# Optimization experiments

Measured on AMD Instinct MI355X. Metric: run time of the kernel, lower is better.

Reference implementation:

```python
import jax, jax.numpy as jnp
from jax import lax
import numpy as np

B, S, MEL = 64, 1024, 60
H, L = 180, 4
FS = 3          # mel_smooth_filter_size (num shifted conv branches)
BLOCKS = 3      # mel_smooth_layers
G = MEL // FS   # 20 output units per grouped conv
POST, OUT = 8192, 300


def setup_inputs() -> dict:
    key = jax.random.key(0)
    ks = jax.random.split(key, 13)
    rn = lambda k, shape, s: jax.random.normal(k, shape, jnp.float32) * s
    x = jax.random.normal(ks[0], (B, S, MEL), jnp.float32)
    lens = jax.random.randint(ks[1], (B,), 1, S + 1)
    conv_w = rn(ks[2], (BLOCKS, FS, G, FS, 5), 0.2)   # per block, per shift: (O=20, I/g=3, k=5)
    conv_b = rn(ks[3], (BLOCKS, FS, G), 0.1)
    lstm_wih0 = rn(ks[4], (4 * H, MEL), 0.08)
    lstm_wih_rest = rn(ks[5], (L - 1, 4 * H, H), 0.08)
    lstm_whh = rn(ks[6], (L, 4 * H, H), 0.08)
    lstm_bih = rn(ks[7], (L, 4 * H), 0.05)
    lstm_bhh = rn(ks[8], (L, 4 * H), 0.05)
    post_w = rn(ks[9], (POST, H), 0.05)
    post_b = rn(ks[10], (POST,), 0.05)
    up_w = rn(ks[11], (OUT, POST), 0.02)
    up_b = rn(ks[12], (OUT,), 0.02)
    return dict(x=x, lens=lens, conv_w=conv_w, conv_b=conv_b,
                lstm_wih0=lstm_wih0, lstm_wih_rest=lstm_wih_rest, lstm_whh=lstm_whh,
                lstm_bih=lstm_bih, lstm_bhh=lstm_bhh,
                post_w=post_w, post_b=post_b, up_w=up_w, up_b=up_b)


def _mel_block(xc, w, b):
    # xc: (B, MEL, S); w: (FS, G, FS, 5); b: (FS, G)
    zrow = jnp.zeros_like(xc[:, :1])
    xs = []
    for i in range(FS - 2):  # shift channels down by i+1
        n = i + 1
        xs.append(jnp.concatenate([jnp.zeros_like(xc[:, :n]), xc[:, :-n]], axis=1))
    xs.append(xc)
    xs.append(jnp.concatenate([xc[:, 1:], zrow], axis=1))  # shift channels up by 1
    outs = []
    for j in range(FS):
        o = lax.conv_general_dilated(xs[j], w[j], (1,), [(2, 2)],
                                     dimension_numbers=('NCH', 'OIH', 'NCH'),
                                     feature_group_count=G)
        outs.append(o + b[j][None, :, None])  # (B, G, S)
    # interleave: out channel FS*i + j = outs[j][:, i]
    return jnp.stack(outs, axis=2).reshape(xc.shape[0], MEL, xc.shape[2])


def _lstm_layer(h_in, wih, whh, bih, bhh):
    # h_in: (B, T, I). Torch gate order: i, f, g, o.
    pre = jnp.einsum('bti,gi->btg', h_in, wih) + (bih + bhh)  # (B, T, 4H)
    pre = pre.transpose(1, 0, 2)  # (T, B, 4H)
    h0 = jnp.zeros((h_in.shape[0], H), h_in.dtype)

    def step(carry, p):
        hh, cc = carry
        gates = p + hh @ whh.T
        i, f, g, o = jnp.split(gates, 4, axis=-1)
        cc = jax.nn.sigmoid(f) * cc + jax.nn.sigmoid(i) * jnp.tanh(g)
        hh = jax.nn.sigmoid(o) * jnp.tanh(cc)
        return (hh, cc), hh

    _, outs = lax.scan(step, (h0, h0), pre)
    return outs.transpose(1, 0, 2)  # (B, T, H)


def reference(x, lens, conv_w, conv_b, lstm_wih0, lstm_wih_rest, lstm_whh,
              lstm_bih, lstm_bhh, post_w, post_b, up_w, up_b):
    xc = x.transpose(0, 2, 1)  # (B, MEL, S)
    for blk in range(BLOCKS):
        shortcut = xc
        xc = _mel_block(xc, conv_w[blk], conv_b[blk]) + shortcut  # resid activation = Identity
    h = xc.transpose(0, 2, 1)  # (B, S, MEL)
    for l in range(L):
        wih = lstm_wih0 if l == 0 else lstm_wih_rest[l - 1]
        h = _lstm_layer(h, wih, lstm_whh[l], lstm_bih[l], lstm_bhh[l])
    idx = jnp.clip(lens - 1, 0, S - 1)
    last = h[jnp.arange(h.shape[0]), idx]  # (B, H)
    post = jax.nn.leaky_relu(last @ post_w.T + post_b, 0.01)  # LeakyReLU default slope
    return post @ up_w.T + up_b  # (B, OUT)
```

## Files before the change

### kernel.cpp

```cpp
#include <hip/hip_runtime.h>
#include <hip/hip_fp16.h>

#define BB 64
#define SS 1024
#define MEL 60
#define HH 180
#define G4 720
#define G4P 768
#define NCG 48
#define NKS 6
#define KP 192
#define NL 4
#define NPOST 8192
#define NOUT 300
#define NOUTP 320
#define KSPL 16
#define TT 128
#define CH 64
#define NCH (SS / CH)
#define KPAIR 96

typedef _Float16 f16x8 __attribute__((ext_vector_type(8)));
typedef float f32x4 __attribute__((ext_vector_type(4)));

#if defined(__has_builtin)
#if __has_builtin(__builtin_amdgcn_fdot2)
#define HAVE_FDOT2 1
#endif
#endif
#ifndef HAVE_FDOT2
#define HAVE_FDOT2 0
#endif

__device__ __forceinline__ float fdot2u(unsigned int w, unsigned int h, float acc) {
#if HAVE_FDOT2
    typedef _Float16 h2_t __attribute__((ext_vector_type(2)));
    union U { unsigned int u; h2_t v; };
    U a, b;
    a.u = w; b.u = h;
    return __builtin_amdgcn_fdot2(a.v, b.v, acc, false);
#else
    __half2 aw = *reinterpret_cast<const __half2*>(&w);
    __half2 ah = *reinterpret_cast<const __half2*>(&h);
    acc += __half2float(__low2half(aw)) * __half2float(__low2half(ah));
    acc += __half2float(__high2half(aw)) * __half2float(__high2half(ah));
    return acc;
#endif
}

union WU { uint4 u; f16x8 f; };

__global__ void prep_wmf(const float* __restrict__ whh, uint4* __restrict__ wmf) {
    int idx = blockIdx.x * blockDim.x + threadIdx.x;
    int total = NL * NCG * NKS * 64;
    if (idx >= total) return;
    int l = idx / (NCG * NKS * 64);
    int r = idx % (NCG * NKS * 64);
    int cg = r / (NKS * 64);
    int r2 = r % (NKS * 64);
    int ks = r2 / 64, lane = r2 % 64;
    int col = cg * 16 + (lane & 15);
    unsigned short v[8];
    #pragma unroll
    for (int j = 0; j < 8; ++j) {
        int k = ks * 32 + ((lane >> 4) << 3) + j;
        float f = (k < HH && col < G4) ? whh[((size_t)l * G4 + col) * HH + k] : 0.f;
        v[j] = __half_as_ushort(__float2half(f));
    }
    uint4 u;
    u.x = (unsigned)v[0] | ((unsigned)v[1] << 16);
    u.y = (unsigned)v[2] | ((unsigned)v[3] << 16);
    u.z = (unsigned)v[4] | ((unsigned)v[5] << 16);
    u.w = (unsigned)v[6] | ((unsigned)v[7] << 16);
    wmf[idx] = u;
}

__global__ void prep_wih16(const float* __restrict__ wih0, const float* __restrict__ wih_rest,
                           unsigned int* __restrict__ w) {
    int idx = blockIdx.x * blockDim.x + threadIdx.x;
    int total = NL * G4 * KPAIR;
    if (idx >= total) return;
    int l = idx / (G4 * KPAIR);
    int r = idx % (G4 * KPAIR);
    int g = r / KPAIR, kp = r % KPAIR;
    int K = (l == 0) ? MEL : HH;
    const float* src = (l == 0) ? (wih0 + (size_t)g * MEL)
                                : (wih_rest + ((size_t)(l - 1) * G4 + g) * HH);
    float a = 0.f, b = 0.f;
    if (2 * kp < K) { a = src[2 * kp]; b = src[2 * kp + 1]; }
    __half2 h2 = __floats2half2_rn(a, b);
    w[idx] = *(unsigned int*)&h2;
}

__global__ void prep_bsum(const float* __restrict__ bih, const float* __restrict__ bhh,
                          float* __restrict__ bsum) {
    int idx = blockIdx.x * blockDim.x + threadIdx.x;
    if (idx >= NL * G4) return;
    bsum[idx] = bih[idx] + bhh[idx];
}

template <typename TIN>
__global__ __launch_bounds__(256) void mel_block(const TIN* __restrict__ in,
                                                 __half* __restrict__ out,
                                                 const float* __restrict__ w,
                                                 const float* __restrict__ bias) {
    __shared__ float xt[TT + 4][MEL];
    __shared__ float ws[900];
    __shared__ float bs[MEL];
    int bb = blockIdx.x;
    int t0 = blockIdx.y * TT;
    int tid = threadIdx.x;
    const TIN* inb = in + (size_t)bb * SS * MEL;
    for (int idx = tid; idx < (TT + 4) * MEL; idx += 256) {
        int tt = idx / MEL, ch = idx % MEL;
        int t = t0 + tt - 2;
        xt[tt][ch] = (t >= 0 && t < SS) ? (float)inb[(size_t)t * MEL + ch] : 0.f;
    }
    for (int idx = tid; idx < 900; idx += 256) ws[idx] = w[idx];
    if (tid < MEL) bs[tid] = bias[(tid % 3) * 20 + tid / 3];
    __syncthreads();
    for (int idx = tid; idx < TT * MEL; idx += 256) {
        int tt = idx / MEL, ch = idx % MEL;
        int i = ch / 3, j = ch % 3;
        int qb = 3 * i + (j - 1);
        float acc = bs[ch];
        #pragma unroll
        for (int c = 0; c < 3; ++c) {
            int q = qb + c;
            if (q >= 0 && q < MEL) {
                const float* wp = ws + ((j * 20 + i) * 3 + c) * 5;
                #pragma unroll
                for (int k = 0; k < 5; ++k) acc += xt[tt + k][q] * wp[k];
            }
        }
        out[(size_t)bb * SS * MEL + (size_t)(t0 + tt) * MEL + ch] =
            __float2half(acc + xt[tt + 2][ch]);
    }
}

struct GemmArgs {
    const __half* A[16];
    const unsigned int* W[16];
    const float* bs[16];
    __half* C[16];
    size_t cbs[16];
    int K[16];
    int KT[16];
    int t0[16];
};

__global__ __launch_bounds__(256) void gemm_pre(GemmArgs ga) {
    int j = blockIdx.z;
    int K = ga.K[j], KT = ga.KT[j];
    const __half* Ab = ga.A[j] + ((size_t)blockIdx.x * SS + ga.t0[j]) * K;
    __half* Cb = ga.C[j] + (size_t)blockIdx.x * ga.cbs[j];
    const unsigned int* Wj = ga.W[j];
    const float* bsum = ga.bs[j];
    __shared__ unsigned int A16[8][72];
    __shared__ unsigned int W16[8][72];
    int n0 = blockIdx.y * 64;
    int tid = threadIdx.x;
    int tx = tid & 15, ty = tid >> 4;
    int kpl = tid & 7, mg = tid >> 3;
    float acc[4][4];
    #pragma unroll
    for (int i = 0; i < 4; ++i)
        #pragma unroll
        for (int jn = 0; jn < 4; ++jn) acc[i][jn] = 0.f;

    for (int kt = 0; kt < KT; ++kt) {
        int kp = kt * 8 + kpl;
        #pragma unroll
        for (int r = 0; r < 2; ++r) {
            int m = mg + 32 * r;
            unsigned int av = 0u;
            if (2 * kp < K) av = *(const unsigned int*)(Ab + (size_t)m * K + 2 * kp);
            A16[kpl][m] = av;
            int g = n0 + m;
            W16[kpl][m] = (g < G4) ? Wj[(size_t)g * KPAIR + kp] : 0u;
        }
        __syncthreads();
        #pragma unroll
        for (int k = 0; k < 8; ++k) {
            unsigned int a[4], b[4];
            #pragma unroll
            for (int i = 0; i < 4; ++i) a[i] = A16[k][ty + (i << 4)];
            #pragma unroll
            for (int jn = 0; jn < 4; ++jn) b[jn] = W16[k][(tx << 2) + jn];
            #pragma unroll
            for (int i = 0; i < 4; ++i)
                #pragma unroll
                for (int jn = 0; jn < 4; ++jn) acc[i][jn] = fdot2u(b[jn], a[i], acc[i][jn]);
        }
        __syncthreads();
    }
    int g0 = n0 + (tx << 2);
    if (g0 < G4) {
        #pragma unroll
        for (int i = 0; i < 4; ++i) {
            int m = ty + (i << 4);
            __half2 p0 = __floats2half2_rn(acc[i][0] + bsum[g0], acc[i][1] + bsum[g0 + 1]);
            __half2 p1 = __floats2half2_rn(acc[i][2] + bsum[g0 + 2], acc[i][3] + bsum[g0 + 3]);
            *(__half2*)(Cb + (size_t)m * G4 + g0) = p0;
            *(__half2*)(Cb + (size_t)m * G4 + g0 + 2) = p1;
        }
    }
}

struct ScanArgs {
    const __half* pre[NL];
    size_t pbs[NL];
    const uint4* wmf[NL];
    __half* hout[NL];
    float* hst[NL];
    float* cst[NL];
    int t0[NL];
};

__global__ __launch_bounds__(768) __attribute__((amdgpu_waves_per_eu(3, 3)))
void lstm_scan(ScanArgs sa) {
    int j = blockIdx.x / BB, b = blockIdx.x % BB;
    int tid = threadIdx.x;
    int wv = tid >> 6, lane = tid & 63;
    int t0 = sa.t0[j];
    const __half* preb = sa.pre[j] + (size_t)b * sa.pbs[j];
    const uint4* wmf = sa.wmf[j];
    __half* houtb = sa.hout[j] + ((size_t)b * SS + (size_t)t0) * HH;
    float* hstb = sa.hst[j] + b * HH;
    float* cstb = sa.cst[j] + b * HH;

    __shared__ __align__(16) unsigned short hs[KP];
    __shared__ float gates[G4P];

    uint4 wfr[24];
    #pragma unroll
    for (int q = 0; q < 4; ++q)
        #pragma unroll
        for (int ks = 0; ks < NKS; ++ks)
            wfr[q * NKS + ks] = wmf[(((size_t)(wv * 4 + q)) * NKS + ks) * 64 + lane];
    #pragma unroll
    for (int r = 0; r < 24; ++r)
        asm volatile("" : "+v"(wfr[r].x), "+v"(wfr[r].y), "+v"(wfr[r].z), "+v"(wfr[r].w));

    float c = 0.f, hlast = 0.f;
    if (tid < KP) {
        float hv = 0.f;
        if (t0 > 0 && tid < HH) { hv = hstb[tid]; c = cstb[tid]; }
        hs[tid] = __half_as_ushort(__float2half(hv));
    }
    __syncthreads();

    float pc0 = 0.f, pc1 = 0.f, pc2 = 0.f, pc3 = 0.f;
    if (tid < HH) {
        pc0 = __half2float(preb[tid]);
        pc1 = __half2float(preb[HH + tid]);
        pc2 = __half2float(preb[2 * HH + tid]);
        pc3 = __half2float(preb[3 * HH + tid]);
    }

    int hoff = (lane >> 4) << 4;
    for (int t = 0; t < CH; ++t) {
        float pn0 = 0.f, pn1 = 0.f, pn2 = 0.f, pn3 = 0.f;
        if (tid < HH && t + 1 < CH) {
            const __half* pp = preb + (size_t)(t + 1) * G4 + tid;
            pn0 = __half2float(pp[0]);
            pn1 = __half2float(pp[HH]);
            pn2 = __half2float(pp[2 * HH]);
            pn3 = __half2float(pp[3 * HH]);
        }
        f16x8 hf[NKS];
        #pragma unroll
        for (int ks = 0; ks < NKS; ++ks) {
            WU hu;
            hu.u = *(const uint4*)((const char*)hs + ks * 64 + hoff);
            hf[ks] = hu.f;
        }
        f32x4 acc0 = {0.f, 0.f, 0.f, 0.f}, acc1 = acc0, acc2 = acc0, acc3 = acc0;
        #pragma unroll
        for (int ks = 0; ks < NKS; ++ks) {
            WU w0, w1, w2, w3;
            w0.u = wfr[0 * NKS + ks]; w1.u = wfr[1 * NKS + ks];
            w2.u = wfr[2 * NKS + ks]; w3.u = wfr[3 * NKS + ks];
            acc0 = __builtin_amdgcn_mfma_f32_16x16x32_f16(hf[ks], w0.f, acc0, 0, 0, 0);
            acc1 = __builtin_amdgcn_mfma_f32_16x16x32_f16(hf[ks], w1.f, acc1, 0, 0, 0);
            acc2 = __builtin_amdgcn_mfma_f32_16x16x32_f16(hf[ks], w2.f, acc2, 0, 0, 0);
            acc3 = __builtin_amdgcn_mfma_f32_16x16x32_f16(hf[ks], w3.f, acc3, 0, 0, 0);
        }
        if (lane < 16) {
            gates[(wv * 4 + 0) * 16 + lane] = acc0[0];
            gates[(wv * 4 + 1) * 16 + lane] = acc1[0];
            gates[(wv * 4 + 2) * 16 + lane] = acc2[0];
            gates[(wv * 4 + 3) * 16 + lane] = acc3[0];
        }
        __syncthreads();
        if (tid < HH) {
            float gi = gates[tid] + pc0;
            float gf = gates[HH + tid] + pc1;
            float gg = gates[2 * HH + tid] + pc2;
            float go = gates[3 * HH + tid] + pc3;
            float si = 1.f / (1.f + __expf(-gi));
            float sf = 1.f / (1.f + __expf(-gf));
            float so = 1.f / (1.f + __expf(-go));
            float tg = 1.f - 2.f / (__expf(2.f * gg) + 1.f);
            c = sf * c + si * tg;
            float hn = so * (1.f - 2.f / (__expf(2.f * c) + 1.f));
            __half hh = __float2half(hn);
            hs[tid] = __half_as_ushort(hh);
            hlast = __half2float(hh);
            houtb[(size_t)t * HH + tid] = hh;
        }
        __syncthreads();
        pc0 = pn0; pc1 = pn1; pc2 = pn2; pc3 = pn3;
    }
    if (tid < HH) { hstb[tid] = hlast; cstb[tid] = c; }
}

__global__ void gather_last(const __half* __restrict__ hfin, const int* __restrict__ lens,
                            float* __restrict__ last) {
    int idx = blockIdx.x * blockDim.x + threadIdx.x;
    if (idx >= BB * HH) return;
    int b = idx / HH, d = idx % HH;
    int t = lens[b] - 1;
    t = t < 0 ? 0 : (t > SS - 1 ? SS - 1 : t);
    last[idx] = __half2float(hfin[((size_t)b * SS + t) * HH + d]);
}

__global__ __launch_bounds__(256) void post_gemm(const float* __restrict__ A,
                                                 const float* __restrict__ Bw,
                                                 const float* __restrict__ pb,
                                                 float* __restrict__ Cb) {
    __shared__ float As[16][68];
    __shared__ float Bs[16][68];
    int n0 = blockIdx.x * 64;
    int tid = threadIdx.x;
    int kk = tid & 15, q = tid >> 4;
    int tx = tid & 15, ty = tid >> 4;
    float acc[4][4];
    #pragma unroll
    for (int i = 0; i < 4; ++i)
        #pragma unroll
        for (int jj = 0; jj < 4; ++jj) acc[i][jj] = 0.f;
    for (int kt = 0; kt < 12; ++kt) {
        int kidx = kt * 16 + kk;
        bool kval = kidx < HH;
        #pragma unroll
        for (int r = 0; r < 4; ++r)
            As[kk][q + (r << 4)] = kval ? A[(size_t)(q + (r << 4)) * HH + kidx] : 0.f;
        #pragma unroll
        for (int r = 0; r < 4; ++r)
            Bs[kk][q + (r << 4)] = kval ? Bw[(size_t)(n0 + q + (r << 4)) * HH + kidx] : 0.f;
        __syncthreads();
        #pragma unroll
        for (int k = 0; k < 16; ++k) {
            float a[4], bv[4];
            #pragma unroll
            for (int i = 0; i < 4; ++i) a[i] = As[k][ty + (i << 4)];
            #pragma unroll
            for (int jj = 0; jj < 4; ++jj) bv[jj] = Bs[k][(tx << 2) + jj];
            #pragma unroll
            for (int i = 0; i < 4; ++i)
                #pragma unroll
                for (int jj = 0; jj < 4; ++jj) acc[i][jj] = fmaf(a[i], bv[jj], acc[i][jj]);
        }
        __syncthreads();
    }
    #pragma unroll
    for (int i = 0; i < 4; ++i) {
        int m = ty + (i << 4);
        #pragma unroll
        for (int jj = 0; jj < 4; ++jj) {
            int g = n0 + (tx << 2) + jj;
            float v = acc[i][jj] + pb[g];
            Cb[(size_t)m * NPOST + g] = v > 0.f ? v : 0.01f * v;
        }
    }
}

__global__ __launch_bounds__(256) void up_gemm(const float* __restrict__ A,
                                               const float* __restrict__ Bw,
                                               float* __restrict__ part) {
    __shared__ float As[16][68];
    __shared__ float Bs[16][68];
    int n0 = blockIdx.x * 64;
    int k0 = blockIdx.y * (NPOST / KSPL);
    float* Pb = part + (size_t)blockIdx.y * BB * NOUTP;
    int tid = threadIdx.x;
    int kk = tid & 15, q = tid >> 4;
    int tx = tid & 15, ty = tid >> 4;
    float acc[4][4];
    #pragma unroll
    for (int i = 0; i < 4; ++i)
        #pragma unroll
        for (int jj = 0; jj < 4; ++jj) acc[i][jj] = 0.f;
    for (int kt = 0; kt < (NPOST / KSPL) / 16; ++kt) {
        int kidx = k0 + kt * 16 + kk;
        #pragma unroll
        for (int r = 0; r < 4; ++r)
            As[kk][q + (r << 4)] = A[(size_t)(q + (r << 4)) * NPOST + kidx];
        #pragma unroll
        for (int r = 0; r < 4; ++r) {
            int g = n0 + q + (r << 4);
            Bs[kk][q + (r << 4)] = (g < NOUT) ? Bw[(size_t)g * NPOST + kidx] : 0.f;
        }
        __syncthreads();
        #pragma unroll
        for (int k = 0; k < 16; ++k) {
            float a[4], bv[4];
            #pragma unroll
            for (int i = 0; i < 4; ++i) a[i] = As[k][ty + (i << 4)];
            #pragma unroll
            for (int jj = 0; jj < 4; ++jj) bv[jj] = Bs[k][(tx << 2) + jj];
            #pragma unroll
            for (int i = 0; i < 4; ++i)
                #pragma unroll
                for (int jj = 0; jj < 4; ++jj) acc[i][jj] = fmaf(a[i], bv[jj], acc[i][jj]);
        }
        __syncthreads();
    }
    #pragma unroll
    for (int i = 0; i < 4; ++i) {
        int m = ty + (i << 4);
        #pragma unroll
        for (int jj = 0; jj < 4; ++jj) {
            int g = n0 + (tx << 2) + jj;
            Pb[(size_t)m * NOUTP + g] = acc[i][jj];
        }
    }
}

__global__ void up_reduce(const float* __restrict__ part, const float* __restrict__ ub,
                          float* __restrict__ out) {
    int idx = blockIdx.x * blockDim.x + threadIdx.x;
    if (idx >= BB * NOUT) return;
    int b = idx / NOUT, o = idx % NOUT;
    float acc = ub[o];
    #pragma unroll
    for (int ks = 0; ks < KSPL; ++ks)
        acc += part[((size_t)ks * BB + b) * NOUTP + o];
    out[(size_t)b * NOUT + o] = acc;
}

extern "C" void kernel_launch(void* const* d_in, const int* in_sizes, int n_in,
                              void* d_out, int out_size, void* d_ws, size_t ws_size,
                              hipStream_t stream) {
    const float* x        = (const float*)d_in[0];
    const int*   lens     = (const int*)d_in[1];
    const float* conv_w   = (const float*)d_in[2];
    const float* conv_b   = (const float*)d_in[3];
    const float* wih0     = (const float*)d_in[4];
    const float* wih_rest = (const float*)d_in[5];
    const float* whh      = (const float*)d_in[6];
    const float* bih      = (const float*)d_in[7];
    const float* bhh      = (const float*)d_in[8];
    const float* post_w   = (const float*)d_in[9];
    const float* post_b   = (const float*)d_in[10];
    const float* up_w     = (const float*)d_in[11];
    const float* up_b     = (const float*)d_in[12];
    float* out = (float*)d_out;
    (void)in_sizes; (void)n_in; (void)out_size;

    auto pad = [](size_t v) { return (v + 255) & ~(size_t)255; };
    const size_t szMel   = (size_t)BB * SS * MEL * 2;
    const size_t szH     = (size_t)BB * SS * HH * 2;
    const size_t szPre0  = (size_t)BB * SS * G4 * 2;
    const size_t szSlot  = (size_t)BB * CH * G4 * 2;
    const size_t szWmf   = (size_t)NL * NCG * NKS * 64 * 16;
    const size_t szWih   = (size_t)NL * G4 * KPAIR * 4;
    const size_t szBsum  = (size_t)NL * G4 * 4;
    const size_t szState = (size_t)NL * BB * HH * 4;
    const size_t szLast  = (size_t)BB * HH * 4;
    const size_t szPost  = (size_t)BB * NPOST * 4;
    const size_t szPart  = (size_t)KSPL * BB * NOUTP * 4;

    size_t commonSmall = pad(szWmf) + pad(szWih) + pad(szBsum) + 2 * pad(szState) +
                         pad(szLast) + pad(szPost) + pad(szPart) + 4096;
    size_t need1 = pad(szMel) + 4 * pad(szH) + pad(szPre0) + 3 * pad(szSlot) + commonSmall;
    size_t need2 = pad(szMel) + 4 * pad(szH) + 4 * pad(szSlot) + commonSmall;
    int tier = (ws_size >= need1) ? 1 : ((ws_size >= need2) ? 2 : 3);

    char* wsp = (char*)d_ws;
    size_t off = 0;
    auto alloc = [&](size_t bytes) -> void* {
        void* p = wsp + off;
        off = (off + bytes + 255) & ~(size_t)255;
        return p;
    };

    __half* melF = (__half*)alloc(szMel);
    __half* hbuf[NL];
    if (tier <= 2) {
        for (int l = 0; l < NL; ++l) hbuf[l] = (__half*)alloc(szH);
    } else {
        __half* p0 = (__half*)alloc(szH);
        __half* p1 = (__half*)alloc(szH);
        hbuf[0] = p0; hbuf[1] = p1; hbuf[2] = p0; hbuf[3] = p1;
    }
    __half* pre0 = nullptr;
    __half* slot[NL] = {nullptr, nullptr, nullptr, nullptr};
    if (tier == 1) {
        pre0 = (__half*)alloc(szPre0);
        for (int l = 1; l < NL; ++l) slot[l] = (__half*)alloc(szSlot);
    } else if (tier == 2) {
        for (int l = 0; l < NL; ++l) slot[l] = (__half*)alloc(szSlot);
    } else {
        slot[0] = (__half*)alloc(szSlot);
        for (int l = 1; l < NL; ++l) slot[l] = slot[0];
    }
    uint4* wmf = (uint4*)alloc(szWmf);
    unsigned int* wih16 = (unsigned int*)alloc(szWih);
    float* bsum  = (float*)alloc(szBsum);
    float* hstates = (float*)alloc(szState);
    float* cstates = (float*)alloc(szState);
    float* lastb = (float*)alloc(szLast);
    float* postb = (float*)alloc(szPost);
    float* partb = (float*)alloc(szPart);

    prep_wmf<<<(NL * NCG * NKS * 64 + 255) / 256, 256, 0, stream>>>(whh, wmf);
    prep_wih16<<<(NL * G4 * KPAIR + 255) / 256, 256, 0, stream>>>(wih0, wih_rest, wih16);
    prep_bsum<<<(NL * G4 + 255) / 256, 256, 0, stream>>>(bih, bhh, bsum);

    {
        __half* m0 = hbuf[0];
        __half* m1 = (__half*)((char*)hbuf[0] + pad(szMel));
        mel_block<float><<<dim3(BB, SS / TT), 256, 0, stream>>>(x, m0, conv_w + 0 * 900, conv_b + 0 * 60);
        mel_block<__half><<<dim3(BB, SS / TT), 256, 0, stream>>>(m0, m1, conv_w + 1 * 900, conv_b + 1 * 60);
        mel_block<__half><<<dim3(BB, SS / TT), 256, 0, stream>>>(m1, melF, conv_w + 2 * 900, conv_b + 2 * 60);
    }

    auto setGemmJob = [&](GemmArgs& ga, int nj, int l, int c) {
        ga.A[nj]  = (l == 0) ? melF : hbuf[l - 1];
        ga.K[nj]  = (l == 0) ? MEL : HH;
        ga.KT[nj] = (l == 0) ? 4 : 12;
        ga.W[nj]  = wih16 + (size_t)l * G4 * KPAIR;
        ga.bs[nj] = bsum + l * G4;
        if (tier == 1 && l == 0) {
            ga.C[nj] = pre0 + (size_t)c * CH * G4;
            ga.cbs[nj] = (size_t)SS * G4;
        } else {
            ga.C[nj] = slot[l];
            ga.cbs[nj] = (size_t)CH * G4;
        }
        ga.t0[nj] = c * CH;
    };
    auto setScanJob = [&](ScanArgs& sa, int nj, int l, int c) {
        if (tier == 1 && l == 0) {
            sa.pre[nj] = pre0 + (size_t)c * CH * G4;
            sa.pbs[nj] = (size_t)SS * G4;
        } else {
            sa.pre[nj] = slot[l];
            sa.pbs[nj] = (size_t)CH * G4;
        }
        sa.wmf[nj]  = wmf + (size_t)l * NCG * NKS * 64;
        sa.hout[nj] = hbuf[l];
        sa.hst[nj]  = hstates + (size_t)l * BB * HH;
        sa.cst[nj]  = cstates + (size_t)l * BB * HH;
        sa.t0[nj]   = c * CH;
    };

    if (tier <= 2) {
        if (tier == 1) {
            GemmArgs ga{};
            for (int c = 0; c < NCH; ++c) setGemmJob(ga, c, 0, c);
            gemm_pre<<<dim3(BB, 12, NCH), 256, 0, stream>>>(ga);
        }
        int lmin = (tier == 1) ? 1 : 0;
        for (int w = 0; w < NCH + NL - 1; ++w) {
            GemmArgs ga{};
            int njg = 0;
            for (int l = lmin; l < NL; ++l) {
                int c = w - l;
                if (c < 0 || c >= NCH) continue;
                setGemmJob(ga, njg++, l, c);
            }
            if (njg) gemm_pre<<<dim3(BB, 12, njg), 256, 0, stream>>>(ga);
            ScanArgs sa{};
            int njs = 0;
            for (int l = 0; l < NL; ++l) {
                int c = w - l;
                if (c < 0 || c >= NCH) continue;
                setScanJob(sa, njs++, l, c);
            }
            if (njs) lstm_scan<<<dim3(njs * BB), 768, 0, stream>>>(sa);
        }
    } else {
        for (int l = 0; l < NL; ++l) {
            for (int c = 0; c < NCH; ++c) {
                GemmArgs ga{}; ScanArgs sa{};
                setGemmJob(ga, 0, l, c);
                gemm_pre<<<dim3(BB, 12, 1), 256, 0, stream>>>(ga);
                setScanJob(sa, 0, l, c);
                lstm_scan<<<dim3(BB), 768, 0, stream>>>(sa);
            }
        }
    }

    gather_last<<<(BB * HH + 255) / 256, 256, 0, stream>>>(hbuf[NL - 1], lens, lastb);
    post_gemm<<<NPOST / 64, 256, 0, stream>>>(lastb, post_w, post_b, postb);
    up_gemm<<<dim3(NOUTP / 64, KSPL), 256, 0, stream>>>(postb, up_w, partb);
    up_reduce<<<(BB * NOUT + 255) / 256, 256, 0, stream>>>(partb, up_b, out);
}
```

Baseline: 2.183 ms.

## Batch 16 sequences per LSTM scan block using full MFMA rows

Restructures the recurrent LSTM scan so each 768-thread block processes 16 batch sequences at once. The hidden state now fills all 16 rows of the MFMA A operand instead of one, and gates are applied in registers with no shared-memory gate exchange. Weights, biases and the pre-activation buffer are re-laid out gate-major and padded so each lane reads its four batch entries contiguously, and the GEMM writes this time-major layout through a shared-memory transpose. This cuts redundant weight-register loads and wasted MFMA rows, but launches only 4 blocks per layer-chunk, so far fewer CUs are busy, and it drops the tier that precomputed layer 0 pre-activations for the whole sequence.

Result: slower. 4.122 ms (+88.8%).

```diff
diff --git a/kernel.cpp b/kernel.cpp
--- a/kernel.cpp
+++ b/kernel.cpp
@@ -6,10 +6,9 @@
 #define MEL 60
 #define HH 180
 #define G4 720
+#define GP 192
 #define G4P 768
-#define NCG 48
 #define NKS 6
-#define KP 192
 #define NL 4
 #define NPOST 8192
 #define NOUT 300
@@ -18,7 +17,7 @@
 #define TT 128
 #define CH 64
 #define NCH (SS / CH)
-#define KPAIR 96
+#define NKP 96
 
 typedef _Float16 f16x8 __attribute__((ext_vector_type(8)));
 typedef float f32x4 __attribute__((ext_vector_type(4)));
@@ -50,21 +49,29 @@
 
 union WU { uint4 u; f16x8 f; };
 
+__device__ __forceinline__ float f16get(uint2 v, int r) {
+    unsigned u = (r < 2) ? v.x : v.y;
+    unsigned short s = (unsigned short)((r & 1) ? (u >> 16) : (u & 0xffffu));
+    return __half2float(__ushort_as_half(s));
+}
+
 __global__ void prep_wmf(const float* __restrict__ whh, uint4* __restrict__ wmf) {
     int idx = blockIdx.x * blockDim.x + threadIdx.x;
-    int total = NL * NCG * NKS * 64;
+    int total = NL * 12 * 4 * NKS * 64;
     if (idx >= total) return;
-    int l = idx / (NCG * NKS * 64);
-    int r = idx % (NCG * NKS * 64);
-    int cg = r / (NKS * 64);
-    int r2 = r % (NKS * 64);
-    int ks = r2 / 64, lane = r2 % 64;
-    int col = cg * 16 + (lane & 15);
+    int l = idx / (12 * 4 * NKS * 64);
+    int r1 = idx % (12 * 4 * NKS * 64);
+    int wv = r1 / (4 * NKS * 64);
+    int r2 = r1 % (4 * NKS * 64);
+    int q = r2 / (NKS * 64);
+    int r3 = r2 % (NKS * 64);
+    int ks = r3 / 64, lane = r3 % 64;
+    int hid = wv * 16 + (lane & 15);
     unsigned short v[8];
     #pragma unroll
     for (int j = 0; j < 8; ++j) {
         int k = ks * 32 + ((lane >> 4) << 3) + j;
-        float f = (k < HH && col < G4) ? whh[((size_t)l * G4 + col) * HH + k] : 0.f;
+        float f = (hid < HH && k < HH) ? whh[((size_t)l * G4 + q * HH + hid) * HH + k] : 0.f;
         v[j] = __half_as_ushort(__float2half(f));
     }
     uint4 u;
@@ -75,28 +82,39 @@
     wmf[idx] = u;
 }
 
-__global__ void prep_wih16(const float* __restrict__ wih0, const float* __restrict__ wih_rest,
-                           unsigned int* __restrict__ w) {
+__global__ void prep_wihP(const float* __restrict__ wih0, const float* __restrict__ wih_rest,
+                          unsigned int* __restrict__ w) {
     int idx = blockIdx.x * blockDim.x + threadIdx.x;
-    int total = NL * G4 * KPAIR;
+    int total = NL * G4P * NKP;
     if (idx >= total) return;
-    int l = idx / (G4 * KPAIR);
-    int r = idx % (G4 * KPAIR);
-    int g = r / KPAIR, kp = r % KPAIR;
+    int l = idx / (G4P * NKP);
+    int r = idx % (G4P * NKP);
+    int col = r / NKP, kp = r % NKP;
+    int q = col / GP, hid = col % GP;
     int K = (l == 0) ? MEL : HH;
-    const float* src = (l == 0) ? (wih0 + (size_t)g * MEL)
-                                : (wih_rest + ((size_t)(l - 1) * G4 + g) * HH);
     float a = 0.f, b = 0.f;
-    if (2 * kp < K) { a = src[2 * kp]; b = src[2 * kp + 1]; }
+    if (hid < HH && 2 * kp < K) {
+        int g = q * HH + hid;
+        const float* src = (l == 0) ? (wih0 + (size_t)g * MEL)
+                                    : (wih_rest + ((size_t)(l - 1) * G4 + g) * HH);
+        a = src[2 * kp]; b = src[2 * kp + 1];
+    }
     __half2 h2 = __floats2half2_rn(a, b);
     w[idx] = *(unsigned int*)&h2;
 }
 
-__global__ void prep_bsum(const float* __restrict__ bih, const float* __restrict__ bhh,
-                          float* __restrict__ bsum) {
+__global__ void prep_bsumP(const float* __restrict__ bih, const float* __restrict__ bhh,
+                           float* __restrict__ bsP) {
     int idx = blockIdx.x * blockDim.x + threadIdx.x;
-    if (idx >= NL * G4) return;
-    bsum[idx] = bih[idx] + bhh[idx];
+    if (idx >= NL * G4P) return;
+    int l = idx / G4P, col = idx % G4P;
+    int q = col / GP, hid = col % GP;
+    float v = 0.f;
+    if (hid < HH) {
+        int g = l * G4 + q * HH + hid;
+        v = bih[g] + bhh[g];
+    }
+    bsP[idx] = v;
 }
 
 template <typename TIN>
@@ -139,26 +157,28 @@
 }
 
 struct GemmArgs {
-    const __half* A[16];
-    const unsigned int* W[16];
-    const float* bs[16];
-    __half* C[16];
-    size_t cbs[16];
-    int K[16];
-    int KT[16];
-    int t0[16];
+    const __half* A[NL];
+    const unsigned int* W[NL];
+    const float* bs[NL];
+    __half* C[NL];
+    int K[NL];
+    int KT[NL];
+    int t0[NL];
 };
 
 __global__ __launch_bounds__(256) void gemm_pre(GemmArgs ga) {
     int j = blockIdx.z;
     int K = ga.K[j], KT = ga.KT[j];
-    const __half* Ab = ga.A[j] + ((size_t)blockIdx.x * SS + ga.t0[j]) * K;
-    __half* Cb = ga.C[j] + (size_t)blockIdx.x * ga.cbs[j];
-    const unsigned int* Wj = ga.W[j];
-    const float* bsum = ga.bs[j];
-    __shared__ unsigned int A16[8][72];
-    __shared__ unsigned int W16[8][72];
+    int tl = blockIdx.x;
+    int tg = ga.t0[j] + tl;
+    const __half* A = ga.A[j];
+    const unsigned int* Wp = ga.W[j];
+    const float* bs = ga.bs[j];
+    __half* Cb = ga.C[j] + (size_t)tl * G4P * BB;
     int n0 = blockIdx.y * 64;
+    __shared__ unsigned int As[8][68];
+    __shared__ unsigned int Ws[8][68];
+    __shared__ __align__(16) unsigned short Ct[64][72];
     int tid = threadIdx.x;
     int tx = tid & 15, ty = tid >> 4;
     int kpl = tid & 7, mg = tid >> 3;
@@ -169,47 +189,49 @@
         for (int jn = 0; jn < 4; ++jn) acc[i][jn] = 0.f;
 
     for (int kt = 0; kt < KT; ++kt) {
-        int kp = kt * 8 + kpl;
+        int kp = (kt << 3) + kpl;
+        bool kv = (2 * kp < K);
         #pragma unroll
         for (int r = 0; r < 2; ++r) {
-            int m = mg + 32 * r;
-            unsigned int av = 0u;
-            if (2 * kp < K) av = *(const unsigned int*)(Ab + (size_t)m * K + 2 * kp);
-            A16[kpl][m] = av;
-            int g = n0 + m;
-            W16[kpl][m] = (g < G4) ? Wj[(size_t)g * KPAIR + kp] : 0u;
+            int b = mg + (r << 5);
+            As[kpl][b] = kv ? *(const unsigned int*)(A + ((size_t)b * SS + tg) * K + 2 * kp) : 0u;
+            Ws[kpl][b] = kv ? Wp[(size_t)(n0 + b) * NKP + kp] : 0u;
         }
         __syncthreads();
         #pragma unroll
         for (int k = 0; k < 8; ++k) {
-            unsigned int a[4], b[4];
-            #pragma unroll
-            for (int i = 0; i < 4; ++i) a[i] = A16[k][ty + (i << 4)];
-            #pragma unroll
-            for (int jn = 0; jn < 4; ++jn) b[jn] = W16[k][(tx << 2) + jn];
+            unsigned int av[4], bv[4];
+            #pragma unroll
+            for (int i = 0; i < 4; ++i) av[i] = As[k][ty + (i << 4)];
+            #pragma unroll
+            for (int jn = 0; jn < 4; ++jn) bv[jn] = Ws[k][(tx << 2) + jn];
             #pragma unroll
             for (int i = 0; i < 4; ++i)
                 #pragma unroll
-                for (int jn = 0; jn < 4; ++jn) acc[i][jn] = fdot2u(b[jn], a[i], acc[i][jn]);
+                for (int jn = 0; jn < 4; ++jn) acc[i][jn] = fdot2u(bv[jn], av[i], acc[i][jn]);
         }
         __syncthreads();
     }
-    int g0 = n0 + (tx << 2);
-    if (g0 < G4) {
-        #pragma unroll
-        for (int i = 0; i < 4; ++i) {
-            int m = ty + (i << 4);
-            __half2 p0 = __floats2half2_rn(acc[i][0] + bsum[g0], acc[i][1] + bsum[g0 + 1]);
-            __half2 p1 = __floats2half2_rn(acc[i][2] + bsum[g0 + 2], acc[i][3] + bsum[g0 + 3]);
-            *(__half2*)(Cb + (size_t)m * G4 + g0) = p0;
-            *(__half2*)(Cb + (size_t)m * G4 + g0 + 2) = p1;
-        }
+    #pragma unroll
+    for (int i = 0; i < 4; ++i) {
+        int b = ty + (i << 4);
+        #pragma unroll
+        for (int jn = 0; jn < 4; ++jn) {
+            int cc = (tx << 2) + jn;
+            float v = acc[i][jn] + bs[n0 + cc];
+            Ct[cc][b] = __half_as_ushort(__float2half(v));
+        }
+    }
+    __syncthreads();
+    for (int w2 = tid; w2 < 64 * 8; w2 += 256) {
+        int rr = w2 >> 3, seg = w2 & 7;
+        uint4 val = *(const uint4*)&Ct[rr][seg << 3];
+        *(uint4*)(Cb + ((size_t)(n0 + rr) * BB + (seg << 3))) = val;
     }
 }
 
 struct ScanArgs {
     const __half* pre[NL];
-    size_t pbs[NL];
     const uint4* wmf[NL];
     __half* hout[NL];
     float* hst[NL];
@@ -219,100 +241,113 @@
 
 __global__ __launch_bounds__(768) __attribute__((amdgpu_waves_per_eu(3, 3)))
 void lstm_scan(ScanArgs sa) {
-    int j = blockIdx.x / BB, b = blockIdx.x % BB;
+    int j = blockIdx.x >> 2, bg = blockIdx.x & 3;
     int tid = threadIdx.x;
     int wv = tid >> 6, lane = tid & 63;
+    int r0 = lane >> 4, cl = lane & 15;
+    int hid = (wv << 4) + cl;
     int t0 = sa.t0[j];
-    const __half* preb = sa.pre[j] + (size_t)b * sa.pbs[j];
-    const uint4* wmf = sa.wmf[j];
-    __half* houtb = sa.hout[j] + ((size_t)b * SS + (size_t)t0) * HH;
-    float* hstb = sa.hst[j] + b * HH;
-    float* cstb = sa.cst[j] + b * HH;
-
-    __shared__ __align__(16) unsigned short hs[KP];
-    __shared__ float gates[G4P];
-
-    uint4 wfr[24];
+    const __half* preb = sa.pre[j];
+    const uint4* wmfw = sa.wmf[j] + (size_t)wv * 4 * NKS * 64;
+    __half* hout = sa.hout[j];
+    float* hst = sa.hst[j];
+    float* cst = sa.cst[j];
+    int b0 = bg << 4;
+    int bl = r0 << 2;
+
+    __shared__ __align__(16) unsigned short hsb[2][16][208];
+
+    uint4 wfr[4][6];
     #pragma unroll
     for (int q = 0; q < 4; ++q)
         #pragma unroll
         for (int ks = 0; ks < NKS; ++ks)
-            wfr[q * NKS + ks] = wmf[(((size_t)(wv * 4 + q)) * NKS + ks) * 64 + lane];
-    #pragma unroll
-    for (int r = 0; r < 24; ++r)
-        asm volatile("" : "+v"(wfr[r].x), "+v"(wfr[r].y), "+v"(wfr[r].z), "+v"(wfr[r].w));
-
-    float c = 0.f, hlast = 0.f;
-    if (tid < KP) {
-        float hv = 0.f;
-        if (t0 > 0 && tid < HH) { hv = hstb[tid]; c = cstb[tid]; }
-        hs[tid] = __half_as_ushort(__float2half(hv));
+            wfr[q][ks] = wmfw[(q * NKS + ks) * 64 + lane];
+    #pragma unroll
+    for (int q = 0; q < 4; ++q)
+        #pragma unroll
+        for (int ks = 0; ks < NKS; ++ks)
+            asm volatile("" : "+v"(wfr[q][ks].x), "+v"(wfr[q][ks].y),
+                              "+v"(wfr[q][ks].z), "+v"(wfr[q][ks].w));
+
+    float c[4] = {0.f, 0.f, 0.f, 0.f};
+    if (t0 > 0) {
+        if (hid < HH) {
+            #pragma unroll
+            for (int r = 0; r < 4; ++r)
+                c[r] = cst[(size_t)(b0 + bl + r) * HH + hid];
+        }
+        for (int idx = tid; idx < 16 * 208; idx += 768) {
+            int b = idx / 208, k = idx % 208;
+            float hv = (k < HH) ? hst[(size_t)(b0 + b) * HH + k] : 0.f;
+            hsb[0][b][k] = __half_as_ushort(__float2half(hv));
+        }
+    } else {
+        for (int idx = tid; idx < 16 * 208; idx += 768)
+            hsb[0][idx / 208][idx % 208] = 0;
     }
     __syncthreads();
 
-    float pc0 = 0.f, pc1 = 0.f, pc2 = 0.f, pc3 = 0.f;
-    if (tid < HH) {
-        pc0 = __half2float(preb[tid]);
-        pc1 = __half2float(preb[HH + tid]);
-        pc2 = __half2float(preb[2 * HH + tid]);
-        pc3 = __half2float(preb[3 * HH + tid]);
-    }
-
-    int hoff = (lane >> 4) << 4;
+    const __half* pl[4];
+    #pragma unroll
+    for (int q = 0; q < 4; ++q)
+        pl[q] = preb + ((size_t)(q * GP + hid) * BB + b0 + bl);
+
+    uint2 pc[4];
+    #pragma unroll
+    for (int q = 0; q < 4; ++q) pc[q] = *(const uint2*)pl[q];
+
+    float hl[4] = {0.f, 0.f, 0.f, 0.f};
     for (int t = 0; t < CH; ++t) {
-        float pn0 = 0.f, pn1 = 0.f, pn2 = 0.f, pn3 = 0.f;
-        if (tid < HH && t + 1 < CH) {
-            const __half* pp = preb + (size_t)(t + 1) * G4 + tid;
-            pn0 = __half2float(pp[0]);
-            pn1 = __half2float(pp[HH]);
-            pn2 = __half2float(pp[2 * HH]);
-            pn3 = __half2float(pp[3 * HH]);
-        }
-        f16x8 hf[NKS];
+        uint2 pn[4] = {{0u,0u},{0u,0u},{0u,0u},{0u,0u}};
+        if (t + 1 < CH) {
+            #pragma unroll
+            for (int q = 0; q < 4; ++q)
+                pn[q] = *(const uint2*)(pl[q] + (size_t)(t + 1) * G4P * BB);
+        }
+        const unsigned short* hrow = hsb[t & 1][cl];
+        f32x4 a0 = {0.f,0.f,0.f,0.f}, a1 = a0, a2 = a0, a3 = a0;
         #pragma unroll
         for (int ks = 0; ks < NKS; ++ks) {
-            WU hu;
-            hu.u = *(const uint4*)((const char*)hs + ks * 64 + hoff);
-            hf[ks] = hu.f;
-        }
-        f32x4 acc0 = {0.f, 0.f, 0.f, 0.f}, acc1 = acc0, acc2 = acc0, acc3 = acc0;
-        #pragma unroll
-        for (int ks = 0; ks < NKS; ++ks) {
+            WU hf;
+            hf.u = *(const uint4*)(hrow + (ks << 5) + (r0 << 3));
             WU w0, w1, w2, w3;
-            w0.u = wfr[0 * NKS + ks]; w1.u = wfr[1 * NKS + ks];
-            w2.u = wfr[2 * NKS + ks]; w3.u = wfr[3 * NKS + ks];
-            acc0 = __builtin_amdgcn_mfma_f32_16x16x32_f16(hf[ks], w0.f, acc0, 0, 0, 0);
-            acc1 = __builtin_amdgcn_mfma_f32_16x16x32_f16(hf[ks], w1.f, acc1, 0, 0, 0);
-            acc2 = __builtin_amdgcn_mfma_f32_16x16x32_f16(hf[ks], w2.f, acc2, 0, 0, 0);
-            acc3 = __builtin_amdgcn_mfma_f32_16x16x32_f16(hf[ks], w3.f, acc3, 0, 0, 0);
-        }
-        if (lane < 16) {
-            gates[(wv * 4 + 0) * 16 + lane] = acc0[0];
-            gates[(wv * 4 + 1) * 16 + lane] = acc1[0];
-            gates[(wv * 4 + 2) * 16 + lane] = acc2[0];
-            gates[(wv * 4 + 3) * 16 + lane] = acc3[0];
-        }
-        __syncthreads();
-        if (tid < HH) {
-            float gi = gates[tid] + pc0;
-            float gf = gates[HH + tid] + pc1;
-            float gg = gates[2 * HH + tid] + pc2;
-            float go = gates[3 * HH + tid] + pc3;
+            w0.u = wfr[0][ks]; w1.u = wfr[1][ks]; w2.u = wfr[2][ks]; w3.u = wfr[3][ks];
+            a0 = __builtin_amdgcn_mfma_f32_16x16x32_f16(hf.f, w0.f, a0, 0, 0, 0);
+            a1 = __builtin_amdgcn_mfma_f32_16x16x32_f16(hf.f, w1.f, a1, 0, 0, 0);
+            a2 = __builtin_amdgcn_mfma_f32_16x16x32_f16(hf.f, w2.f, a2, 0, 0, 0);
+            a3 = __builtin_amdgcn_mfma_f32_16x16x32_f16(hf.f, w3.f, a3, 0, 0, 0);
+        }
+        unsigned short* hnx = &hsb[(t + 1) & 1][0][0];
+        #pragma unroll
+        for (int r = 0; r < 4; ++r) {
+            float gi = a0[r] + f16get(pc[0], r);
+            float gf = a1[r] + f16get(pc[1], r);
+            float gg = a2[r] + f16get(pc[2], r);
+            float go = a3[r] + f16get(pc[3], r);
             float si = 1.f / (1.f + __expf(-gi));
             float sf = 1.f / (1.f + __expf(-gf));
             float so = 1.f / (1.f + __expf(-go));
             float tg = 1.f - 2.f / (__expf(2.f * gg) + 1.f);
-            c = sf * c + si * tg;
-            float hn = so * (1.f - 2.f / (__expf(2.f * c) + 1.f));
+            c[r] = sf * c[r] + si * tg;
+            float hn = so * (1.f - 2.f / (__expf(2.f * c[r]) + 1.f));
+            hl[r] = hn;
             __half hh = __float2half(hn);
-            hs[tid] = __half_as_ushort(hh);
-            hlast = __half2float(hh);
-            houtb[(size_t)t * HH + tid] = hh;
+            hnx[(bl + r) * 208 + hid] = __half_as_ushort(hh);
+            if (hid < HH)
+                hout[((size_t)(b0 + bl + r) * SS + t0 + t) * HH + hid] = hh;
         }
         __syncthreads();
-        pc0 = pn0; pc1 = pn1; pc2 = pn2; pc3 = pn3;
-    }
-    if (tid < HH) { hstb[tid] = hlast; cstb[tid] = c; }
+        #pragma unroll
+        for (int q = 0; q < 4; ++q) pc[q] = pn[q];
+    }
+    if (hid < HH) {
+        #pragma unroll
+        for (int r = 0; r < 4; ++r) {
+            cst[(size_t)(b0 + bl + r) * HH + hid] = c[r];
+            hst[(size_t)(b0 + bl + r) * HH + hid] = hl[r];
+        }
+    }
 }
 
 __global__ void gather_last(const __half* __restrict__ hfin, const int* __restrict__ lens,
@@ -462,21 +497,19 @@
     auto pad = [](size_t v) { return (v + 255) & ~(size_t)255; };
     const size_t szMel   = (size_t)BB * SS * MEL * 2;
     const size_t szH     = (size_t)BB * SS * HH * 2;
-    const size_t szPre0  = (size_t)BB * SS * G4 * 2;
-    const size_t szSlot  = (size_t)BB * CH * G4 * 2;
-    const size_t szWmf   = (size_t)NL * NCG * NKS * 64 * 16;
-    const size_t szWih   = (size_t)NL * G4 * KPAIR * 4;
-    const size_t szBsum  = (size_t)NL * G4 * 4;
-    const size_t szState = (size_t)NL * BB * HH * 4;
+    const size_t szSlot  = (size_t)CH * G4P * BB * 2;
+    const size_t szWmf   = (size_t)NL * 12 * 4 * NKS * 64 * 16;
+    const size_t szWihP  = (size_t)NL * G4P * NKP * 4;
+    const size_t szBsP   = (size_t)NL * G4P * 4;
+    const size_t szState = (size_t)BB * HH * 4;
     const size_t szLast  = (size_t)BB * HH * 4;
     const size_t szPost  = (size_t)BB * NPOST * 4;
     const size_t szPart  = (size_t)KSPL * BB * NOUTP * 4;
 
-    size_t commonSmall = pad(szWmf) + pad(szWih) + pad(szBsum) + 2 * pad(szState) +
+    size_t commonSmall = pad(szWmf) + pad(szWihP) + pad(szBsP) + 2 * NL * pad(szState) +
                          pad(szLast) + pad(szPost) + pad(szPart) + 4096;
-    size_t need1 = pad(szMel) + 4 * pad(szH) + pad(szPre0) + 3 * pad(szSlot) + commonSmall;
-    size_t need2 = pad(szMel) + 4 * pad(szH) + 4 * pad(szSlot) + commonSmall;
-    int tier = (ws_size >= need1) ? 1 : ((ws_size >= need2) ? 2 : 3);
+    size_t needWF = pad(szMel) + 4 * pad(szH) + 4 * pad(szSlot) + commonSmall;
+    int wavefront = (ws_size >= needWF) ? 1 : 0;
 
     char* wsp = (char*)d_ws;
     size_t off = 0;
@@ -488,36 +521,33 @@
 
     __half* melF = (__half*)alloc(szMel);
     __half* hbuf[NL];
-    if (tier <= 2) {
+    if (wavefront) {
         for (int l = 0; l < NL; ++l) hbuf[l] = (__half*)alloc(szH);
     } else {
         __half* p0 = (__half*)alloc(szH);
         __half* p1 = (__half*)alloc(szH);
         hbuf[0] = p0; hbuf[1] = p1; hbuf[2] = p0; hbuf[3] = p1;
     }
-    __half* pre0 = nullptr;
-    __half* slot[NL] = {nullptr, nullptr, nullptr, nullptr};
-    if (tier == 1) {
-        pre0 = (__half*)alloc(szPre0);
-        for (int l = 1; l < NL; ++l) slot[l] = (__half*)alloc(szSlot);
-    } else if (tier == 2) {
+    __half* slot[NL];
+    if (wavefront) {
         for (int l = 0; l < NL; ++l) slot[l] = (__half*)alloc(szSlot);
     } else {
         slot[0] = (__half*)alloc(szSlot);
         for (int l = 1; l < NL; ++l) slot[l] = slot[0];
     }
     uint4* wmf = (uint4*)alloc(szWmf);
-    unsigned int* wih16 = (unsigned int*)alloc(szWih);
-    float* bsum  = (float*)alloc(szBsum);
-    float* hstates = (float*)alloc(szState);
-    float* cstates = (float*)alloc(szState);
+    unsigned int* wihP = (unsigned int*)alloc(szWihP);
+    float* bsP = (float*)alloc(szBsP);
+    float* hstates = (float*)alloc(NL * pad(szState));
+    float* cstates = (float*)alloc(NL * pad(szState));
     float* lastb = (float*)alloc(szLast);
     float* postb = (float*)alloc(szPost);
     float* partb = (float*)alloc(szPart);
-
-    prep_wmf<<<(NL * NCG * NKS * 64 + 255) / 256, 256, 0, stream>>>(whh, wmf);
-    prep_wih16<<<(NL * G4 * KPAIR + 255) / 256, 256, 0, stream>>>(wih0, wih_rest, wih16);
-    prep_bsum<<<(NL * G4 + 255) / 256, 256, 0, stream>>>(bih, bhh, bsum);
+    size_t stStride = pad(szState) / 4;
+
+    prep_wmf<<<(NL * 12 * 4 * NKS * 64 + 255) / 256, 256, 0, stream>>>(whh, wmf);
+    prep_wihP<<<(NL * G4P * NKP + 255) / 256, 256, 0, stream>>>(wih0, wih_rest, wihP);
+    prep_bsumP<<<(NL * G4P + 255) / 256, 256, 0, stream>>>(bih, bhh, bsP);
 
     {
         __half* m0 = hbuf[0];
@@ -531,48 +561,30 @@
         ga.A[nj]  = (l == 0) ? melF : hbuf[l - 1];
         ga.K[nj]  = (l == 0) ? MEL : HH;
         ga.KT[nj] = (l == 0) ? 4 : 12;
-        ga.W[nj]  = wih16 + (size_t)l * G4 * KPAIR;
-        ga.bs[nj] = bsum + l * G4;
-        if (tier == 1 && l == 0) {
-            ga.C[nj] = pre0 + (size_t)c * CH * G4;
-            ga.cbs[nj] = (size_t)SS * G4;
-        } else {
-            ga.C[nj] = slot[l];
-            ga.cbs[nj] = (size_t)CH * G4;
-        }
+        ga.W[nj]  = wihP + (size_t)l * G4P * NKP;
+        ga.bs[nj] = bsP + (size_t)l * G4P;
+        ga.C[nj]  = slot[l];
         ga.t0[nj] = c * CH;
     };
     auto setScanJob = [&](ScanArgs& sa, int nj, int l, int c) {
-        if (tier == 1 && l == 0) {
-            sa.pre[nj] = pre0 + (size_t)c * CH * G4;
-            sa.pbs[nj] = (size_t)SS * G4;
-        } else {
-            sa.pre[nj] = slot[l];
-            sa.pbs[nj] = (size_t)CH * G4;
-        }
-        sa.wmf[nj]  = wmf + (size_t)l * NCG * NKS * 64;
+        sa.pre[nj]  = slot[l];
+        sa.wmf[nj]  = wmf + (size_t)l * 12 * 4 * NKS * 64;
         sa.hout[nj] = hbuf[l];
-        sa.hst[nj]  = hstates + (size_t)l * BB * HH;
-        sa.cst[nj]  = cstates + (size_t)l * BB * HH;
+        sa.hst[nj]  = hstates + (size_t)l * stStride;
+        sa.cst[nj]  = cstates + (size_t)l * stStride;
         sa.t0[nj]   = c * CH;
     };
 
-    if (tier <= 2) {
-        if (tier == 1) {
-            GemmArgs ga{};
-            for (int c = 0; c < NCH; ++c) setGemmJob(ga, c, 0, c);
-            gemm_pre<<<dim3(BB, 12, NCH), 256, 0, stream>>>(ga);
-        }
-        int lmin = (tier == 1) ? 1 : 0;
+    if (wavefront) {
         for (int w = 0; w < NCH + NL - 1; ++w) {
             GemmArgs ga{};
             int njg = 0;
-            for (int l = lmin; l < NL; ++l) {
+            for (int l = 0; l < NL; ++l) {
                 int c = w - l;
                 if (c < 0 || c >= NCH) continue;
                 setGemmJob(ga, njg++, l, c);
             }
-            if (njg) gemm_pre<<<dim3(BB, 12, njg), 256, 0, stream>>>(ga);
+            if (njg) gemm_pre<<<dim3(CH, 12, njg), 256, 0, stream>>>(ga);
             ScanArgs sa{};
             int njs = 0;
             for (int l = 0; l < NL; ++l) {
@@ -580,16 +592,16 @@
                 if (c < 0 || c >= NCH) continue;
                 setScanJob(sa, njs++, l, c);
             }
-            if (njs) lstm_scan<<<dim3(njs * BB), 768, 0, stream>>>(sa);
+            if (njs) lstm_scan<<<dim3(njs * 4), 768, 0, stream>>>(sa);
         }
     } else {
         for (int l = 0; l < NL; ++l) {
             for (int c = 0; c < NCH; ++c) {
                 GemmArgs ga{}; ScanArgs sa{};
                 setGemmJob(ga, 0, l, c);
-                gemm_pre<<<dim3(BB, 12, 1), 256, 0, stream>>>(ga);
+                gemm_pre<<<dim3(CH, 12, 1), 256, 0, stream>>>(ga);
                 setScanJob(sa, 0, l, c);
-                lstm_scan<<<dim3(BB), 768, 0, stream>>>(sa);
+                lstm_scan<<<dim3(4), 768, 0, stream>>>(sa);
             }
         }
     }
```

## Gate-aligned weight layout so each wave computes LSTM cell update in registers

Applied to the files above, without the earlier changes.

The recurrent weight fragments are reordered so that each wave's four MFMA accumulators hold the i, f, g, o gates for the same 16 hidden units. The cell update can then be done directly from the accumulators, with no shared-memory gates buffer. The hidden-state buffer is double-buffered, which removes one of the two barriers per timestep on the serial LSTM critical path. The cost is that every lane now runs the activation math, including lanes whose results are redundant or inactive.

New measurement: 2.453 ms. 12.4% more time.

```diff
diff --git a/kernel.cpp b/kernel.cpp
--- a/kernel.cpp
+++ b/kernel.cpp
@@ -6,8 +6,6 @@
 #define MEL 60
 #define HH 180
 #define G4 720
-#define G4P 768
-#define NCG 48
 #define NKS 6
 #define KP 192
 #define NL 4
@@ -52,19 +50,20 @@
 
 __global__ void prep_wmf(const float* __restrict__ whh, uint4* __restrict__ wmf) {
     int idx = blockIdx.x * blockDim.x + threadIdx.x;
-    int total = NL * NCG * NKS * 64;
+    int total = NL * 48 * NKS * 64;
     if (idx >= total) return;
-    int l = idx / (NCG * NKS * 64);
-    int r = idx % (NCG * NKS * 64);
-    int cg = r / (NKS * 64);
-    int r2 = r % (NKS * 64);
+    int l = idx / (48 * NKS * 64);
+    int r1 = idx % (48 * NKS * 64);
+    int g = r1 / (NKS * 64);
+    int r2 = r1 % (NKS * 64);
     int ks = r2 / 64, lane = r2 % 64;
-    int col = cg * 16 + (lane & 15);
+    int q = g / 12, hg = g % 12;
+    int hid = hg * 16 + (lane & 15);
     unsigned short v[8];
     #pragma unroll
     for (int j = 0; j < 8; ++j) {
         int k = ks * 32 + ((lane >> 4) << 3) + j;
-        float f = (k < HH && col < G4) ? whh[((size_t)l * G4 + col) * HH + k] : 0.f;
+        float f = (hid < HH && k < HH) ? whh[((size_t)l * G4 + q * HH + hid) * HH + k] : 0.f;
         v[j] = __half_as_ushort(__float2half(f));
     }
     uint4 u;
@@ -222,97 +221,98 @@
     int j = blockIdx.x / BB, b = blockIdx.x % BB;
     int tid = threadIdx.x;
     int wv = tid >> 6, lane = tid & 63;
+    int r0 = lane >> 4, cl = lane & 15;
+    int hid = (wv << 4) + cl;
     int t0 = sa.t0[j];
     const __half* preb = sa.pre[j] + (size_t)b * sa.pbs[j];
-    const uint4* wmf = sa.wmf[j];
     __half* houtb = sa.hout[j] + ((size_t)b * SS + (size_t)t0) * HH;
     float* hstb = sa.hst[j] + b * HH;
     float* cstb = sa.cst[j] + b * HH;
-
-    __shared__ __align__(16) unsigned short hs[KP];
-    __shared__ float gates[G4P];
-
-    uint4 wfr[24];
+    bool act = (hid < HH);
+
+    __shared__ __align__(16) unsigned short hs[2][KP];
+
+    uint4 wfr[4][NKS];
+    {
+        const uint4* wm = sa.wmf[j];
+        #pragma unroll
+        for (int q = 0; q < 4; ++q)
+            #pragma unroll
+            for (int ks = 0; ks < NKS; ++ks)
+                wfr[q][ks] = wm[((q * 12 + wv) * NKS + ks) * 64 + lane];
+    }
     #pragma unroll
     for (int q = 0; q < 4; ++q)
         #pragma unroll
         for (int ks = 0; ks < NKS; ++ks)
-            wfr[q * NKS + ks] = wmf[(((size_t)(wv * 4 + q)) * NKS + ks) * 64 + lane];
-    #pragma unroll
-    for (int r = 0; r < 24; ++r)
-        asm volatile("" : "+v"(wfr[r].x), "+v"(wfr[r].y), "+v"(wfr[r].z), "+v"(wfr[r].w));
-
-    float c = 0.f, hlast = 0.f;
+            asm volatile("" : "+v"(wfr[q][ks].x), "+v"(wfr[q][ks].y),
+                              "+v"(wfr[q][ks].z), "+v"(wfr[q][ks].w));
+
+    float c = 0.f, hl = 0.f;
+    if (t0 > 0 && act) c = cstb[hid];
     if (tid < KP) {
         float hv = 0.f;
-        if (t0 > 0 && tid < HH) { hv = hstb[tid]; c = cstb[tid]; }
-        hs[tid] = __half_as_ushort(__float2half(hv));
+        if (t0 > 0 && tid < HH) hv = hstb[tid];
+        hs[0][tid] = __half_as_ushort(__float2half(hv));
     }
     __syncthreads();
 
-    float pc0 = 0.f, pc1 = 0.f, pc2 = 0.f, pc3 = 0.f;
-    if (tid < HH) {
-        pc0 = __half2float(preb[tid]);
-        pc1 = __half2float(preb[HH + tid]);
-        pc2 = __half2float(preb[2 * HH + tid]);
-        pc3 = __half2float(preb[3 * HH + tid]);
-    }
-
-    int hoff = (lane >> 4) << 4;
+    float pc[4] = {0.f, 0.f, 0.f, 0.f};
+    if (act) {
+        #pragma unroll
+        for (int q = 0; q < 4; ++q) pc[q] = __half2float(preb[q * HH + hid]);
+    }
+    int hoff = r0 << 4;
     for (int t = 0; t < CH; ++t) {
-        float pn0 = 0.f, pn1 = 0.f, pn2 = 0.f, pn3 = 0.f;
-        if (tid < HH && t + 1 < CH) {
-            const __half* pp = preb + (size_t)(t + 1) * G4 + tid;
-            pn0 = __half2float(pp[0]);
-            pn1 = __half2float(pp[HH]);
-            pn2 = __half2float(pp[2 * HH]);
-            pn3 = __half2float(pp[3 * HH]);
-        }
+        float pn[4] = {0.f, 0.f, 0.f, 0.f};
+        if (act && t + 1 < CH) {
+            const __half* pp = preb + (size_t)(t + 1) * G4;
+            #pragma unroll
+            for (int q = 0; q < 4; ++q) pn[q] = __half2float(pp[q * HH + hid]);
+        }
+        const unsigned short* hrow = hs[t & 1];
         f16x8 hf[NKS];
         #pragma unroll
         for (int ks = 0; ks < NKS; ++ks) {
             WU hu;
-            hu.u = *(const uint4*)((const char*)hs + ks * 64 + hoff);
+            hu.u = *(const uint4*)((const char*)hrow + (ks << 6) + hoff);
             hf[ks] = hu.f;
         }
-        f32x4 acc0 = {0.f, 0.f, 0.f, 0.f}, acc1 = acc0, acc2 = acc0, acc3 = acc0;
+        f32x4 a0 = {0.f,0.f,0.f,0.f}, a1 = a0, a2 = a0, a3 = a0;
         #pragma unroll
         for (int ks = 0; ks < NKS; ++ks) {
             WU w0, w1, w2, w3;
-            w0.u = wfr[0 * NKS + ks]; w1.u = wfr[1 * NKS + ks];
-            w2.u = wfr[2 * NKS + ks]; w3.u = wfr[3 * NKS + ks];
-            acc0 = __builtin_amdgcn_mfma_f32_16x16x32_f16(hf[ks], w0.f, acc0, 0, 0, 0);
-            acc1 = __builtin_amdgcn_mfma_f32_16x16x32_f16(hf[ks], w1.f, acc1, 0, 0, 0);
-            acc2 = __builtin_amdgcn_mfma_f32_16x16x32_f16(hf[ks], w2.f, acc2, 0, 0, 0);
-            acc3 = __builtin_amdgcn_mfma_f32_16x16x32_f16(hf[ks], w3.f, acc3, 0, 0, 0);
-        }
-        if (lane < 16) {
-            gates[(wv * 4 + 0) * 16 + lane] = acc0[0];
-            gates[(wv * 4 + 1) * 16 + lane] = acc1[0];
-            gates[(wv * 4 + 2) * 16 + lane] = acc2[0];
-            gates[(wv * 4 + 3) * 16 + lane] = acc3[0];
+            w0.u = wfr[0][ks]; w1.u = wfr[1][ks]; w2.u = wfr[2][ks]; w3.u = wfr[3][ks];
+            a0 = __builtin_amdgcn_mfma_f32_16x16x32_f16(hf[ks], w0.f, a0, 0, 0, 0);
+            a1 = __builtin_amdgcn_mfma_f32_16x16x32_f16(hf[ks], w1.f, a1, 0, 0, 0);
+            a2 = __builtin_amdgcn_mfma_f32_16x16x32_f16(hf[ks], w2.f, a2, 0, 0, 0);
+            a3 = __builtin_amdgcn_mfma_f32_16x16x32_f16(hf[ks], w3.f, a3, 0, 0, 0);
+        }
+        float gi = a0[0] + pc[0];
+        float gf = a1[0] + pc[1];
+        float gg = a2[0] + pc[2];
+        float go = a3[0] + pc[3];
+        float si = 1.f / (1.f + __expf(-gi));
+        float sf = 1.f / (1.f + __expf(-gf));
+        float so = 1.f / (1.f + __expf(-go));
+        float tg = 1.f - 2.f / (__expf(2.f * gg) + 1.f);
+        c = sf * c + si * tg;
+        float hn = so * (1.f - 2.f / (__expf(2.f * c) + 1.f));
+        if (!act) hn = 0.f;
+        hl = hn;
+        __half hh = __float2half(hn);
+        if (r0 == 0) {
+            hs[(t + 1) & 1][hid] = __half_as_ushort(hh);
+            if (act) houtb[(size_t)t * HH + hid] = hh;
         }
         __syncthreads();
-        if (tid < HH) {
-            float gi = gates[tid] + pc0;
-            float gf = gates[HH + tid] + pc1;
-            float gg = gates[2 * HH + tid] + pc2;
-            float go = gates[3 * HH + tid] + pc3;
-            float si = 1.f / (1.f + __expf(-gi));
-            float sf = 1.f / (1.f + __expf(-gf));
-            float so = 1.f / (1.f + __expf(-go));
-            float tg = 1.f - 2.f / (__expf(2.f * gg) + 1.f);
-            c = sf * c + si * tg;
-            float hn = so * (1.f - 2.f / (__expf(2.f * c) + 1.f));
-            __half hh = __float2half(hn);
-            hs[tid] = __half_as_ushort(hh);
-            hlast = __half2float(hh);
-            houtb[(size_t)t * HH + tid] = hh;
-        }
-        __syncthreads();
-        pc0 = pn0; pc1 = pn1; pc2 = pn2; pc3 = pn3;
-    }
-    if (tid < HH) { hstb[tid] = hlast; cstb[tid] = c; }
+        #pragma unroll
+        for (int q = 0; q < 4; ++q) pc[q] = pn[q];
+    }
+    if (r0 == 0 && act) {
+        cstb[hid] = c;
+        hstb[hid] = hl;
+    }
 }
 
 __global__ void gather_last(const __half* __restrict__ hfin, const int* __restrict__ lens,
@@ -464,7 +464,7 @@
     const size_t szH     = (size_t)BB * SS * HH * 2;
     const size_t szPre0  = (size_t)BB * SS * G4 * 2;
     const size_t szSlot  = (size_t)BB * CH * G4 * 2;
-    const size_t szWmf   = (size_t)NL * NCG * NKS * 64 * 16;
+    const size_t szWmf   = (size_t)NL * 48 * NKS * 64 * 16;
     const size_t szWih   = (size_t)NL * G4 * KPAIR * 4;
     const size_t szBsum  = (size_t)NL * G4 * 4;
     const size_t szState = (size_t)NL * BB * HH * 4;
@@ -515,7 +515,7 @@
     float* postb = (float*)alloc(szPost);
     float* partb = (float*)alloc(szPart);
 
-    prep_wmf<<<(NL * NCG * NKS * 64 + 255) / 256, 256, 0, stream>>>(whh, wmf);
+    prep_wmf<<<(NL * 48 * NKS * 64 + 255) / 256, 256, 0, stream>>>(whh, wmf);
     prep_wih16<<<(NL * G4 * KPAIR + 255) / 256, 256, 0, stream>>>(wih0, wih_rest, wih16);
     prep_bsum<<<(NL * G4 + 255) / 256, 256, 0, stream>>>(bih, bhh, bsum);
 
@@ -550,7 +550,7 @@
             sa.pre[nj] = slot[l];
             sa.pbs[nj] = (size_t)CH * G4;
         }
-        sa.wmf[nj]  = wmf + (size_t)l * NCG * NKS * 64;
+        sa.wmf[nj]  = wmf + (size_t)l * 48 * NKS * 64;
         sa.hout[nj] = hbuf[l];
         sa.hst[nj]  = hstates + (size_t)l * BB * HH;
         sa.cst[nj]  = cstates + (size_t)l * BB * HH;
```
